# Kernel tuning notes

Hardware: AMD Instinct MI355X
Metric: run time of the kernel (lower is better)

## Reference

```python
import jax, jax.numpy as jnp
import numpy as np

N = 100000        # nodes
E = 1600000       # edges (before self loops)
IN_DIM = 128
OUT_DIM = 64
HEADS = 4
CH = OUT_DIM // HEADS   # 16 channels per head
G = 64            # graphs in batch
EPS = 1e-5        # GraphNorm eps
SLOPE = 0.2       # LeakyReLU negative slope (GATv2Conv default)


def setup_inputs() -> dict:
    key = jax.random.key(0)
    ks = jax.random.split(key, 8)
    x = jax.random.normal(ks[0], (N, IN_DIM), dtype=jnp.float32)
    edge_index = jax.random.randint(ks[1], (2, E), 0, N, dtype=jnp.int64)
    batch = jnp.sort(jax.random.randint(ks[2], (N,), 0, G, dtype=jnp.int64))
    s_in = 1.0 / np.sqrt(IN_DIM)
    # GATv2Conv params (share_weights=False): W_l for source, W_r for target
    Wl = jax.random.normal(ks[3], (IN_DIM, HEADS * CH), dtype=jnp.float32) * s_in
    Wr = jax.random.normal(ks[4], (IN_DIM, HEADS * CH), dtype=jnp.float32) * s_in
    att = jax.random.normal(ks[5], (HEADS, CH), dtype=jnp.float32) * (1.0 / np.sqrt(CH))
    conv_bias = jnp.zeros((HEADS * CH,), dtype=jnp.float32)
    # skip Linear
    skip_W = jax.random.normal(ks[6], (IN_DIM, OUT_DIM), dtype=jnp.float32) * s_in
    skip_b = jax.random.normal(ks[7], (OUT_DIM,), dtype=jnp.float32) * s_in
    # GraphNorm params (PyG init: weight=1, bias=0, mean_scale=1)
    ones = jnp.ones((OUT_DIM,), dtype=jnp.float32)
    zeros = jnp.zeros((OUT_DIM,), dtype=jnp.float32)
    return {
        "x": x, "edge_index": edge_index, "batch": batch,
        "Wl": Wl, "Wr": Wr, "att": att, "conv_bias": conv_bias,
        "skip_W": skip_W, "skip_b": skip_b,
        "bn_w": ones, "bn_b": zeros, "bn_ms": ones,
        "sn_w": ones, "sn_b": zeros, "sn_ms": ones,
    }


def _gatv2(x, Wl, Wr, att, bias, src, dst):
    n = x.shape[0]
    xl = (x @ Wl).reshape(n, HEADS, CH)   # source transform (also the message)
    xr = (x @ Wr).reshape(n, HEADS, CH)   # target transform
    # GATv2: score = a . LeakyReLU(xl[j] + xr[i]) per head
    e = jax.nn.leaky_relu(xl[src] + xr[dst], SLOPE)          # [E,H,C]
    score = jnp.einsum('ehc,hc->eh', e, att)                  # [E,H]
    # segment softmax over edges sharing a target node
    smax = jax.ops.segment_max(score, dst, num_segments=n)    # [N,H]
    ex = jnp.exp(score - smax[dst])
    denom = jax.ops.segment_sum(ex, dst, num_segments=n)
    alpha = ex / denom[dst]                                   # [E,H]
    out = jax.ops.segment_sum(xl[src] * alpha[:, :, None], dst, num_segments=n)
    return out.reshape(n, HEADS * CH) + bias


def _graph_norm(x, w, b, ms, batch):
    cnt = jax.ops.segment_sum(jnp.ones((x.shape[0],), x.dtype), batch, num_segments=G)
    cnt = jnp.maximum(cnt, 1.0)[:, None]
    mean = jax.ops.segment_sum(x, batch, num_segments=G) / cnt
    cen = x - mean[batch] * ms
    var = jax.ops.segment_sum(cen * cen, batch, num_segments=G) / cnt
    inv = jax.lax.rsqrt(var + EPS)
    return w * cen * inv[batch] + b


def reference(x, edge_index, batch, Wl, Wr, att, conv_bias, skip_W, skip_b,
              bn_w, bn_b, bn_ms, sn_w, sn_b, sn_ms):
    n = x.shape[0]
    loop = jnp.arange(n, dtype=edge_index.dtype)  # add_self_loops=True default
    src = jnp.concatenate([edge_index[0], loop])
    dst = jnp.concatenate([edge_index[1], loop])
    x_main = _gatv2(x, Wl, Wr, att, conv_bias, src, dst)
    x_main = _graph_norm(x_main, bn_w, bn_b, bn_ms, batch)
    x_skip = _graph_norm(x @ skip_W + skip_b, sn_w, sn_b, sn_ms, batch)
    return jax.nn.elu(x_main + x_skip)
```

## Files before the change

kernel.cpp:

```cpp
#include <hip/hip_runtime.h>

#define IND 128
#define OUTD 64
#define NG 64
#define NPART 8
#define NSTRIPE 256
#define SLOPE 0.2f
#define EPSV 1e-5f
#define JMASK 131071
#define DEGCAP 48
#define NSB (NG * NPART)
#define GSLOT 4

typedef short bf16x8 __attribute__((ext_vector_type(8)));
typedef float f32x4 __attribute__((ext_vector_type(4)));
typedef float f32x2 __attribute__((ext_vector_type(2)));

__device__ __forceinline__ unsigned bf16rne(float f) {
  unsigned u = __float_as_uint(f);
  return (u + 0x7fffu + ((u >> 16) & 1u)) >> 16;
}
__device__ __forceinline__ unsigned pack2(float a, float b) {
  return bf16rne(a) | (bf16rne(b) << 16);
}
__device__ __forceinline__ unsigned pack2u(unsigned a, unsigned b) {
  return pack2(__uint_as_float(a), __uint_as_float(b));
}

__device__ __forceinline__ void gload_lds16(const void* g, void* l) {
  __builtin_amdgcn_global_load_lds(
      (const __attribute__((address_space(1))) void*)g,
      (__attribute__((address_space(3))) void*)l, 16, 0, 2);
}

__global__ __launch_bounds__(256) void wcvt_kernel(
    const float* __restrict__ Wl, const float* __restrict__ Wr,
    const float* __restrict__ Ws, unsigned short* __restrict__ wt) {
  int i = blockIdx.x * 256 + threadIdx.x;
  if (i >= 3 * 64 * 128) return;
  int k = i & 127, col = (i >> 7) & 63, which = i >> 13;
  const float* W = (which == 0) ? Wl : (which == 1) ? Wr : Ws;
  int p = col >> 1, odd = col & 1;
  int m = p & 15, h = p >> 4;
  int t = which * 4 + 2 * h + odd;
  int kc = k >> 5, quad = (k >> 3) & 3, j = k & 7;
  int slot = ((t * 4 + kc) * 4 + quad) * 16 + m;
  wt[slot * 8 + j] = (unsigned short)bf16rne(W[k * OUTD + col]);
}

__device__ __forceinline__ void gemm3_body(
    int bx, const float* __restrict__ x, const unsigned short* __restrict__ wt,
    const float* __restrict__ skip_b,
    unsigned* __restrict__ xlb, unsigned* __restrict__ xrb,
    unsigned* __restrict__ xsb,
    int n, uint4* ldsx) {
  int tid = threadIdx.x;
  int wave = tid >> 6, lane = tid & 63;
  int m = lane & 15, quad = lane >> 4;

#pragma unroll
  for (int i = 0; i < 8; ++i) {
    int c = i * 256 + tid;
    int row = c >> 5, u = c & 31;
    int us = u ^ (row & 7);
    int growc = min(bx * 64 + row, n - 1);
    gload_lds16(x + (size_t)growc * IND + us * 4, &ldsx[c]);
  }
  __syncthreads();

  int lbase = (wave * 16 + m) * 32;
  int swz = m & 7;
  union { uint4 u; bf16x8 v; } af[4];
#pragma unroll
  for (int kc = 0; kc < 4; ++kc) {
    int u0 = kc * 8 + quad * 2;
    uint4 A0 = ldsx[lbase + (u0 ^ swz)];
    uint4 A1 = ldsx[lbase + ((u0 + 1) ^ swz)];
    af[kc].u = make_uint4(pack2u(A0.x, A0.y), pack2u(A0.z, A0.w),
                          pack2u(A1.x, A1.y), pack2u(A1.z, A1.w));
  }

  f32x4 acc[12] = {};
#pragma unroll
  for (int kc = 0; kc < 4; ++kc) {
#pragma unroll
    for (int t = 0; t < 12; ++t) {
      const bf16x8* bp =
          (const bf16x8*)&wt[(((t * 4 + kc) * 4 + quad) * 16 + m) * 8];
      acc[t] = __builtin_amdgcn_mfma_f32_16x16x32_bf16(af[kc].v, *bp, acc[t], 0, 0, 0);
    }
  }

  float sb0[2], sb1[2];
#pragma unroll
  for (int h = 0; h < 2; ++h) {
    sb0[h] = skip_b[h * 32 + 2 * m];
    sb1[h] = skip_b[h * 32 + 2 * m + 1];
  }

  int orow_base = bx * 64 + wave * 16 + quad * 4;
#pragma unroll
  for (int r = 0; r < 4; ++r) {
    int orow = orow_base + r;
    bool ok = orow < n;
    int wbase = (orow << 5) + m;
#pragma unroll
    for (int h = 0; h < 2; ++h) {
      if (ok) xlb[wbase + h * 16] = pack2(acc[2 * h][r], acc[2 * h + 1][r]);
    }
#pragma unroll
    for (int h = 0; h < 2; ++h) {
      if (ok) xrb[wbase + h * 16] = pack2(acc[4 + 2 * h][r], acc[5 + 2 * h][r]);
    }
#pragma unroll
    for (int h = 0; h < 2; ++h) {
      if (ok) xsb[wbase + h * 16] = pack2(acc[8 + 2 * h][r] + sb0[h],
                                          acc[9 + 2 * h][r] + sb1[h]);
    }
  }
}

__device__ __forceinline__ void scat1(int d, int s, int lo, int hi,
                                      int* count, int* __restrict__ bucket) {
  if (d >= lo && d < hi) {
    int p = atomicAdd(&count[d], 1);
    if (p < DEGCAP) bucket[d * DEGCAP + p] = s;
  }
}

__device__ __forceinline__ void scatter_body(int r, int stripe,
                                             const int* __restrict__ src,
                                             const int* __restrict__ dst,
                                             int* count, int* __restrict__ bucket,
                                             int E, int n8) {
  int lo = r * n8, hi = lo + n8;
  int per = (((E + NSTRIPE - 1) / NSTRIPE) + 3) & ~3;
  int s0 = stripe * per;
  int s1 = min(E, s0 + per);
  for (int e = s0 + (int)threadIdx.x * 4; e < s1; e += 1024) {
    if (e + 4 <= s1) {
      int4 d4 = *(const int4*)&dst[e];
      int4 s4 = *(const int4*)&src[e];
      scat1(d4.x, s4.x, lo, hi, count, bucket);
      scat1(d4.y, s4.y, lo, hi, count, bucket);
      scat1(d4.z, s4.z, lo, hi, count, bucket);
      scat1(d4.w, s4.w, lo, hi, count, bucket);
    } else {
      for (int q = e; q < s1; ++q)
        scat1(dst[q], src[q], lo, hi, count, bucket);
    }
  }
}

__device__ __forceinline__ void goff_body(int bx, const int* __restrict__ batch,
                                          int* goff, int n) {
  int i = bx * 256 + threadIdx.x;
  if (i >= n) return;
  int b = batch[i];
  int prev = (i == 0) ? -1 : batch[i - 1];
  for (int g = prev + 1; g <= b; ++g) goff[g] = i;
  if (i == n - 1)
    for (int g = b + 1; g <= NG; ++g) goff[g] = n;
}

__global__ __launch_bounds__(256) void mega1_kernel(
    const float* __restrict__ x, const unsigned short* __restrict__ wt,
    const float* __restrict__ skip_b,
    unsigned* __restrict__ xlb, unsigned* __restrict__ xrb,
    unsigned* __restrict__ xsb,
    const int* __restrict__ src, const int* __restrict__ dst,
    int* count, int* bucket,
    const int* __restrict__ batch, int* goff,
    int n, int E, int n8, int nbG, int nbB, int SG, int GG) {
  __shared__ uint4 ldsx[2048];
  int group = blockIdx.x >> 3, pos = blockIdx.x & 7;
  int gtot = SG + GG;
  int before = (int)(((long long)group * SG) / gtot);
  int after  = (int)(((long long)(group + 1) * SG) / gtot);
  if (after > before) {
    scatter_body(pos, before, src, dst, count, bucket, E, n8);
  } else {
    int g = (group - before) * 8 + pos;
    if (g < nbG) gemm3_body(g, x, wt, skip_b, xlb, xrb, xsb, n, ldsx);
    else if (g < nbG + nbB) goff_body(g - nbG, batch, goff, n);
  }
}

__global__ __launch_bounds__(256) void edge_kernel(
    const unsigned* __restrict__ xlb, const unsigned* __restrict__ xrb,
    const int* __restrict__ count, const int* __restrict__ bucket,
    const float* __restrict__ att, const float* __restrict__ conv_bias,
    const unsigned* __restrict__ xsb, const int* __restrict__ goff,
    float* __restrict__ part,
    float* __restrict__ out_main, int n) {
  int tid = threadIdx.x;
  int bxr = (int)blockIdx.x;

  if (bxr < NSB) {
    int g = bxr >> 3, q = bxr & 7;
    int start = goff[g], end = goff[g + 1];
    int col = tid & 63, grp = tid >> 6;
    float s1s = 0.f, s2s = 0.f;
    for (int node = start + q * 4 + grp; node < end; node += 4 * NPART) {
      unsigned w2 = __builtin_nontemporal_load(&xsb[(node << 5) | (col >> 1)]);
      float vs = __uint_as_float((col & 1) ? (w2 & 0xffff0000u) : (w2 << 16));
      s1s += vs; s2s += vs * vs;
    }
    __shared__ float red[2][4][64];
    red[0][grp][col] = s1s; red[1][grp][col] = s2s;
    __syncthreads();
    if (tid < 64) {
      float* dstp = &part[(g * NPART + q) * 256 + 128];
#pragma unroll
      for (int st = 0; st < 2; ++st) {
        float s = red[st][0][tid] + red[st][1][tid] + red[st][2][tid] +
                  red[st][3][tid];
        dstp[st * 64 + tid] = s;
      }
    }
    return;
  }

  int bx = bxr - NSB;
  int wave = tid >> 6;
  int lane = tid & 63;
  int half = lane >> 5;
  int sub = lane & 31;
  int node = bx * 8 + wave * 2 + half;
  bool act = node < n;
  int nodec = min(node, n - 1);
  int base2 = (nodec << 6) | (sub << 1);

  unsigned ur = __builtin_nontemporal_load(&xrb[(nodec << 5) | sub]);
  float xrc0 = __uint_as_float(ur << 16);
  float xrc1 = __uint_as_float(ur & 0xffff0000u);
  unsigned us = xlb[(nodec << 5) | sub];
  float xs0 = __uint_as_float(us << 16);
  float xs1 = __uint_as_float(us & 0xffff0000u);
  float2 att2 = *(const float2*)&att[sub << 1];

  float t0 = xs0 + xrc0, t1 = xs1 + xrc1;
  t0 = fmaxf(t0, SLOPE * t0);
  t1 = fmaxf(t1, SLOPE * t1);
  float s = t0 * att2.x + t1 * att2.y;
  s += __shfl_xor(s, 1);
  s += __shfl_xor(s, 2);
  s += __shfl_xor(s, 4);
  const float sself = s;

  int e0 = nodec * DEGCAP;
  int deg = min(count[nodec], DEGCAP);
  int iters = max(deg, __shfl_xor(deg, 32));

  float denom = 1.f;
  float a0 = xs0, a1 = xs1;
  int i = 0;
  for (; i + 7 < iters; i += 8) {
    float p[8], v0[8], v1[8];
#pragma unroll
    for (int k = 0; k < 8; ++k) {
      bool a = (i + k < deg);
      int e = a ? (e0 + i + k) : e0;
      int j = bucket[e] & JMASK;
      unsigned u = xlb[(j << 5) | sub];
      v0[k] = __uint_as_float(u << 16);
      v1[k] = __uint_as_float(u & 0xffff0000u);
      float tx = v0[k] + xrc0, ty = v1[k] + xrc1;
      tx = fmaxf(tx, SLOPE * tx); ty = fmaxf(ty, SLOPE * ty);
      float sc = tx * att2.x + ty * att2.y;
      sc += __shfl_xor(sc, 1);
      sc += __shfl_xor(sc, 2);
      sc += __shfl_xor(sc, 4);
      p[k] = a ? __expf(sc - sself) : 0.f;
    }
#pragma unroll
    for (int k = 0; k < 8; ++k) {
      denom += p[k];
      a0 += p[k] * v0[k];
      a1 += p[k] * v1[k];
    }
  }
  for (; i < iters; ++i) {
    bool a = (i < deg);
    int e = a ? (e0 + i) : e0;
    int j = bucket[e] & JMASK;
    unsigned u = xlb[(j << 5) | sub];
    float v0 = __uint_as_float(u << 16);
    float v1 = __uint_as_float(u & 0xffff0000u);
    float tx = v0 + xrc0, ty = v1 + xrc1;
    tx = fmaxf(tx, SLOPE * tx); ty = fmaxf(ty, SLOPE * ty);
    float sc = tx * att2.x + ty * att2.y;
    sc += __shfl_xor(sc, 1);
    sc += __shfl_xor(sc, 2);
    sc += __shfl_xor(sc, 4);
    float p = a ? __expf(sc - sself) : 0.f;
    denom += p;
    a0 += p * v0;
    a1 += p * v1;
  }
  float inv = 1.f / denom;
  float2 cb = *(const float2*)&conv_bias[sub << 1];
  if (act) {
    f32x2 o; o.x = a0 * inv + cb.x; o.y = a1 * inv + cb.y;
    __builtin_nontemporal_store(o, (f32x2*)&out_main[base2]);
  }
}

__global__ __launch_bounds__(256) void stats_part_kernel(
    const float* __restrict__ mainv,
    const int* __restrict__ goff, float* __restrict__ part) {
  int g = blockIdx.x, q = blockIdx.y;
  int start = goff[g], end = goff[g + 1];
  int col = threadIdx.x & 63, grp = threadIdx.x >> 6;
  float s1m = 0.f, s2m = 0.f;
  for (int node = start + q * 4 + grp; node < end; node += 4 * NPART) {
    float vm = __builtin_nontemporal_load(&mainv[(node << 6) | col]);
    s1m += vm; s2m += vm * vm;
  }
  __shared__ float red[2][4][64];
  red[0][grp][col] = s1m; red[1][grp][col] = s2m;
  __syncthreads();
  if (threadIdx.x < 64) {
    int c = threadIdx.x;
    float* dst = &part[(g * NPART + q) * 256];
#pragma unroll
    for (int st = 0; st < 2; ++st) {
      float s = red[st][0][c] + red[st][1][c] + red[st][2][c] + red[st][3][c];
      dst[st * 64 + c] = s;
    }
  }
}

__global__ __launch_bounds__(256) void final_kernel(
    const unsigned* __restrict__ xsb, const int* __restrict__ batch,
    const float* __restrict__ part, const int* __restrict__ goff,
    const float* __restrict__ bn_w, const float* __restrict__ bn_b,
    const float* __restrict__ bn_ms,
    const float* __restrict__ sn_w, const float* __restrict__ sn_b,
    const float* __restrict__ sn_ms,
    float* out, int n) {
  __shared__ float A1s[GSLOT][64], B1s[GSLOT][64];
  __shared__ float A2s[GSLOT][64], B2s[GSLOT][64];
  int b = blockIdx.x;
  int tid = threadIdx.x;
  int node0 = b * 16;
  int nodeH = min(node0 + 15, n - 1);
  int gL = batch[node0];
  int gH = batch[nodeH];
  int ng = gH - gL + 1;

  int slot = tid >> 6, c = tid & 63;
  if (slot < ng && slot < GSLOT) {
    int g = gL + slot;
    float S1m = 0.f, S2m = 0.f, S1s = 0.f, S2s = 0.f;
    for (int q = 0; q < NPART; ++q) {
      const float* p = &part[(g * NPART + q) * 256];
      S1m += p[c];       S2m += p[64 + c];
      S1s += p[128 + c]; S2s += p[192 + c];
    }
    float cnt = fmaxf((float)(goff[g + 1] - goff[g]), 1.f);
    float meanM = S1m / cnt;
    float aM = meanM * bn_ms[c];
    float varM = S2m / cnt - 2.f * aM * meanM + aM * aM;
    float invM = rsqrtf(varM + EPSV);
    float am = bn_w[c] * invM;
    A1s[slot][c] = am;
    B1s[slot][c] = bn_b[c] - am * aM;
    float meanS = S1s / cnt;
    float aS = meanS * sn_ms[c];
    float varS = S2s / cnt - 2.f * aS * meanS + aS * aS;
    float invS = rsqrtf(varS + EPSV);
    float as_ = sn_w[c] * invS;
    A2s[slot][c] = as_;
    B2s[slot][c] = sn_b[c] - as_ * aS;
  }
  __syncthreads();

  int idx = b * 256 + tid;
  if (idx >= n * 16) return;
  int node = idx >> 4;
  int c4 = (idx & 15) << 2;
  int sl = min(batch[node] - gL, GSLOT - 1);
  f32x4 mv = __builtin_nontemporal_load((const f32x4*)&out[idx << 2]);
  uint2 sw = *(const uint2*)&xsb[(node << 5) + (c4 >> 1)];
  float sv0 = __uint_as_float(sw.x << 16);
  float sv1 = __uint_as_float(sw.x & 0xffff0000u);
  float sv2 = __uint_as_float(sw.y << 16);
  float sv3 = __uint_as_float(sw.y & 0xffff0000u);
  f32x4 v;
  v.x = A1s[sl][c4 + 0] * mv.x + B1s[sl][c4 + 0] + A2s[sl][c4 + 0] * sv0 + B2s[sl][c4 + 0];
  v.y = A1s[sl][c4 + 1] * mv.y + B1s[sl][c4 + 1] + A2s[sl][c4 + 1] * sv1 + B2s[sl][c4 + 1];
  v.z = A1s[sl][c4 + 2] * mv.z + B1s[sl][c4 + 2] + A2s[sl][c4 + 2] * sv2 + B2s[sl][c4 + 2];
  v.w = A1s[sl][c4 + 3] * mv.w + B1s[sl][c4 + 3] + A2s[sl][c4 + 3] * sv3 + B2s[sl][c4 + 3];
  v.x = (v.x > 0.f) ? v.x : (__expf(v.x) - 1.f);
  v.y = (v.y > 0.f) ? v.y : (__expf(v.y) - 1.f);
  v.z = (v.z > 0.f) ? v.z : (__expf(v.z) - 1.f);
  v.w = (v.w > 0.f) ? v.w : (__expf(v.w) - 1.f);
  __builtin_nontemporal_store(v, (f32x4*)&out[idx << 2]);
}

extern "C" void kernel_launch(void* const* d_in, const int* in_sizes, int n_in,
                              void* d_out, int out_size, void* d_ws, size_t ws_size,
                              hipStream_t stream) {
  const float* x        = (const float*)d_in[0];
  const int*   ei       = (const int*)d_in[1];
  const int*   batch    = (const int*)d_in[2];
  const float* Wl       = (const float*)d_in[3];
  const float* Wr       = (const float*)d_in[4];
  const float* att      = (const float*)d_in[5];
  const float* conv_b   = (const float*)d_in[6];
  const float* skip_W   = (const float*)d_in[7];
  const float* skip_b   = (const float*)d_in[8];
  const float* bn_w     = (const float*)d_in[9];
  const float* bn_b     = (const float*)d_in[10];
  const float* bn_ms    = (const float*)d_in[11];
  const float* sn_w     = (const float*)d_in[12];
  const float* sn_b     = (const float*)d_in[13];
  const float* sn_ms    = (const float*)d_in[14];

  int n = in_sizes[0] / IND;
  int E = in_sizes[1] / 2;
  const int* src = ei;
  const int* dst = ei + E;
  float* out = (float*)d_out;

  char* w = (char*)d_ws;
  int* count  = (int*)w;   w += (size_t)(n + 64) * 4;
  int* goff   = (int*)w;   w += (size_t)(NG + 64) * 4;
  float* part = (float*)w; w += (size_t)NG * NPART * 256 * 4;
  unsigned short* wt = (unsigned short*)w; w += (size_t)3 * 64 * IND * 2;
  int* bucket = (int*)w;   w += (size_t)n * DEGCAP * 4;
  unsigned* xlb = (unsigned*)w; w += (size_t)n * 32 * 4;
  unsigned* xrb = (unsigned*)w; w += (size_t)n * 32 * 4;
  unsigned* xsb = (unsigned*)w; w += (size_t)n * 32 * 4;

  int n8 = (n + 7) / 8;
  int nbG = (n + 63) / 64;
  int nbB = (n + 255) / 256;
  int SG = NSTRIPE;
  int GG = (nbG + nbB + 7) / 8;

  (void)hipMemsetAsync(count, 0, (size_t)(n + 1) * 4, stream);

  wcvt_kernel<<<(3 * 64 * IND + 255) / 256, 256, 0, stream>>>(Wl, Wr, skip_W, wt);

  mega1_kernel<<<8 * (SG + GG), 256, 0, stream>>>(
      x, wt, skip_b, xlb, xrb, xsb, src, dst, count, bucket, batch, goff,
      n, E, n8, nbG, nbB, SG, GG);

  edge_kernel<<<NSB + (n + 7) / 8, 256, 0, stream>>>(
      xlb, xrb, count, bucket, att, conv_b, xsb, goff, part, out, n);

  dim3 sg(NG, NPART);
  stats_part_kernel<<<sg, 256, 0, stream>>>(out, goff, part);
  final_kernel<<<(n * 16 + 255) / 256, 256, 0, stream>>>(
      xsb, batch, part, goff, bn_w, bn_b, bn_ms, sn_w, sn_b, sn_ms, out, n);
}
```

Baseline: 311.8 us.

## Store GAT conv output as bf16 intermediate and vectorize GEMM output stores

The edge kernel now writes the attention-aggregated conv output as packed bf16 into a new workspace buffer instead of fp32 into the output. The stats and final kernels read that buffer, which halves intermediate traffic. Separately, the weight layout is reordered so each lane owns four consecutive columns, letting the GEMM epilogue write 8-byte uint2 stores and load the skip bias as one vector. The cost is an extra rounding of the pre-norm activations to bf16, which reduces accuracy.

```diff
diff --git a/kernel.cpp b/kernel.cpp
--- a/kernel.cpp
+++ b/kernel.cpp
@@ -40,9 +40,8 @@
   if (i >= 3 * 64 * 128) return;
   int k = i & 127, col = (i >> 7) & 63, which = i >> 13;
   const float* W = (which == 0) ? Wl : (which == 1) ? Wr : Ws;
-  int p = col >> 1, odd = col & 1;
-  int m = p & 15, h = p >> 4;
-  int t = which * 4 + 2 * h + odd;
+  int m = col >> 2;
+  int t = which * 4 + (col & 3);
   int kc = k >> 5, quad = (k >> 3) & 3, j = k & 7;
   int slot = ((t * 4 + kc) * 4 + quad) * 16 + m;
   wt[slot * 8 + j] = (unsigned short)bf16rne(W[k * OUTD + col]);
@@ -91,31 +90,24 @@
     }
   }
 
-  float sb0[2], sb1[2];
-#pragma unroll
-  for (int h = 0; h < 2; ++h) {
-    sb0[h] = skip_b[h * 32 + 2 * m];
-    sb1[h] = skip_b[h * 32 + 2 * m + 1];
-  }
+  f32x4 sb = *(const f32x4*)&skip_b[4 * m];
 
   int orow_base = bx * 64 + wave * 16 + quad * 4;
 #pragma unroll
   for (int r = 0; r < 4; ++r) {
     int orow = orow_base + r;
     bool ok = orow < n;
-    int wbase = (orow << 5) + m;
-#pragma unroll
-    for (int h = 0; h < 2; ++h) {
-      if (ok) xlb[wbase + h * 16] = pack2(acc[2 * h][r], acc[2 * h + 1][r]);
-    }
-#pragma unroll
-    for (int h = 0; h < 2; ++h) {
-      if (ok) xrb[wbase + h * 16] = pack2(acc[4 + 2 * h][r], acc[5 + 2 * h][r]);
-    }
-#pragma unroll
-    for (int h = 0; h < 2; ++h) {
-      if (ok) xsb[wbase + h * 16] = pack2(acc[8 + 2 * h][r] + sb0[h],
-                                          acc[9 + 2 * h][r] + sb1[h]);
+    int wbase = (orow << 5) + 2 * m;
+    if (ok) {
+      uint2 vl; vl.x = pack2(acc[0][r], acc[1][r]);
+      vl.y = pack2(acc[2][r], acc[3][r]);
+      *(uint2*)&xlb[wbase] = vl;
+      uint2 vr; vr.x = pack2(acc[4][r], acc[5][r]);
+      vr.y = pack2(acc[6][r], acc[7][r]);
+      *(uint2*)&xrb[wbase] = vr;
+      uint2 vs; vs.x = pack2(acc[8][r] + sb.x, acc[9][r] + sb.y);
+      vs.y = pack2(acc[10][r] + sb.z, acc[11][r] + sb.w);
+      *(uint2*)&xsb[wbase] = vs;
     }
   }
 }
@@ -192,7 +184,7 @@
     const float* __restrict__ att, const float* __restrict__ conv_bias,
     const unsigned* __restrict__ xsb, const int* __restrict__ goff,
     float* __restrict__ part,
-    float* __restrict__ out_main, int n) {
+    unsigned* __restrict__ outb, int n) {
   int tid = threadIdx.x;
   int bxr = (int)blockIdx.x;
 
@@ -229,7 +221,6 @@
   int node = bx * 8 + wave * 2 + half;
   bool act = node < n;
   int nodec = min(node, n - 1);
-  int base2 = (nodec << 6) | (sub << 1);
 
   unsigned ur = __builtin_nontemporal_load(&xrb[(nodec << 5) | sub]);
   float xrc0 = __uint_as_float(ur << 16);
@@ -301,20 +292,21 @@
   float inv = 1.f / denom;
   float2 cb = *(const float2*)&conv_bias[sub << 1];
   if (act) {
-    f32x2 o; o.x = a0 * inv + cb.x; o.y = a1 * inv + cb.y;
-    __builtin_nontemporal_store(o, (f32x2*)&out_main[base2]);
+    unsigned w2 = pack2(a0 * inv + cb.x, a1 * inv + cb.y);
+    __builtin_nontemporal_store(w2, &outb[(nodec << 5) | sub]);
   }
 }
 
 __global__ __launch_bounds__(256) void stats_part_kernel(
-    const float* __restrict__ mainv,
+    const unsigned* __restrict__ outb,
     const int* __restrict__ goff, float* __restrict__ part) {
   int g = blockIdx.x, q = blockIdx.y;
   int start = goff[g], end = goff[g + 1];
   int col = threadIdx.x & 63, grp = threadIdx.x >> 6;
   float s1m = 0.f, s2m = 0.f;
   for (int node = start + q * 4 + grp; node < end; node += 4 * NPART) {
-    float vm = __builtin_nontemporal_load(&mainv[(node << 6) | col]);
+    unsigned w2 = __builtin_nontemporal_load(&outb[(node << 5) | (col >> 1)]);
+    float vm = __uint_as_float((col & 1) ? (w2 & 0xffff0000u) : (w2 << 16));
     s1m += vm; s2m += vm * vm;
   }
   __shared__ float red[2][4][64];
@@ -332,7 +324,8 @@
 }
 
 __global__ __launch_bounds__(256) void final_kernel(
-    const unsigned* __restrict__ xsb, const int* __restrict__ batch,
+    const unsigned* __restrict__ xsb, const unsigned* __restrict__ outb,
+    const int* __restrict__ batch,
     const float* __restrict__ part, const int* __restrict__ goff,
     const float* __restrict__ bn_w, const float* __restrict__ bn_b,
     const float* __restrict__ bn_ms,
@@ -381,17 +374,21 @@
   int node = idx >> 4;
   int c4 = (idx & 15) << 2;
   int sl = min(batch[node] - gL, GSLOT - 1);
-  f32x4 mv = __builtin_nontemporal_load((const f32x4*)&out[idx << 2]);
+  uint2 mw = *(const uint2*)&outb[(node << 5) + (c4 >> 1)];
+  float mv0 = __uint_as_float(mw.x << 16);
+  float mv1 = __uint_as_float(mw.x & 0xffff0000u);
+  float mv2 = __uint_as_float(mw.y << 16);
+  float mv3 = __uint_as_float(mw.y & 0xffff0000u);
   uint2 sw = *(const uint2*)&xsb[(node << 5) + (c4 >> 1)];
   float sv0 = __uint_as_float(sw.x << 16);
   float sv1 = __uint_as_float(sw.x & 0xffff0000u);
   float sv2 = __uint_as_float(sw.y << 16);
   float sv3 = __uint_as_float(sw.y & 0xffff0000u);
   f32x4 v;
-  v.x = A1s[sl][c4 + 0] * mv.x + B1s[sl][c4 + 0] + A2s[sl][c4 + 0] * sv0 + B2s[sl][c4 + 0];
-  v.y = A1s[sl][c4 + 1] * mv.y + B1s[sl][c4 + 1] + A2s[sl][c4 + 1] * sv1 + B2s[sl][c4 + 1];
-  v.z = A1s[sl][c4 + 2] * mv.z + B1s[sl][c4 + 2] + A2s[sl][c4 + 2] * sv2 + B2s[sl][c4 + 2];
-  v.w = A1s[sl][c4 + 3] * mv.w + B1s[sl][c4 + 3] + A2s[sl][c4 + 3] * sv3 + B2s[sl][c4 + 3];
+  v.x = A1s[sl][c4 + 0] * mv0 + B1s[sl][c4 + 0] + A2s[sl][c4 + 0] * sv0 + B2s[sl][c4 + 0];
+  v.y = A1s[sl][c4 + 1] * mv1 + B1s[sl][c4 + 1] + A2s[sl][c4 + 1] * sv1 + B2s[sl][c4 + 1];
+  v.z = A1s[sl][c4 + 2] * mv2 + B1s[sl][c4 + 2] + A2s[sl][c4 + 2] * sv2 + B2s[sl][c4 + 2];
+  v.w = A1s[sl][c4 + 3] * mv3 + B1s[sl][c4 + 3] + A2s[sl][c4 + 3] * sv3 + B2s[sl][c4 + 3];
   v.x = (v.x > 0.f) ? v.x : (__expf(v.x) - 1.f);
   v.y = (v.y > 0.f) ? v.y : (__expf(v.y) - 1.f);
   v.z = (v.z > 0.f) ? v.z : (__expf(v.z) - 1.f);
@@ -433,6 +430,7 @@
   unsigned* xlb = (unsigned*)w; w += (size_t)n * 32 * 4;
   unsigned* xrb = (unsigned*)w; w += (size_t)n * 32 * 4;
   unsigned* xsb = (unsigned*)w; w += (size_t)n * 32 * 4;
+  unsigned* outb = (unsigned*)w; w += (size_t)n * 32 * 4;
 
   int n8 = (n + 7) / 8;
   int nbG = (n + 63) / 64;
@@ -449,10 +447,11 @@
       n, E, n8, nbG, nbB, SG, GG);
 
   edge_kernel<<<NSB + (n + 7) / 8, 256, 0, stream>>>(
-      xlb, xrb, count, bucket, att, conv_b, xsb, goff, part, out, n);
+      xlb, xrb, count, bucket, att, conv_b, xsb, goff, part, outb, n);
 
   dim3 sg(NG, NPART);
-  stats_part_kernel<<<sg, 256, 0, stream>>>(out, goff, part);
+  stats_part_kernel<<<sg, 256, 0, stream>>>(outb, goff, part);
   final_kernel<<<(n * 16 + 255) / 256, 256, 0, stream>>>(
-      xsb, batch, part, goff, bn_w, bn_b, bn_ms, sn_w, sn_b, sn_ms, out, n);
-}
+      xsb, outb, batch, part, goff, bn_w, bn_b, bn_ms, sn_w, sn_b, sn_ms,
+      out, n);
+}
```

New measurement: 314.3 us. About the same (+0.8%).
